# Kernel tuning notes

Hardware: AMD Instinct MI355X
Metric: run time of the kernel (lower is better)

## Reference

```python
import jax, jax.numpy as jnp
import numpy as np

NUM_CLASSES = 15
NUM_ANCHORS = 18          # 3 anchor sizes x 6 angles
STRIDE = 8
SCALE_XY = 1.05


def setup_inputs() -> dict:
    key = jax.random.key(0)
    B, G = 16, 64
    output = jax.random.normal(key, (B, NUM_ANCHORS * (NUM_CLASSES + 6), G, G), dtype=jnp.float32)
    anchors = [(12.0, 16.0), (19.0, 36.0), (40.0, 28.0)]
    angles = [-np.pi / 3, -np.pi / 6, 0.0, np.pi / 6, np.pi / 3, np.pi / 2]
    ma = np.array([(w / STRIDE, h / STRIDE, a) for (w, h) in anchors for a in angles], dtype=np.float32)
    return {"output": output, "masked_anchors": jnp.asarray(ma)}


def reference(output, masked_anchors):
    B, _, G, _ = output.shape
    # [B, nA, G, G, 6+C]
    pred = output.reshape(B, NUM_ANCHORS, NUM_CLASSES + 6, G, G).transpose(0, 1, 3, 4, 2)

    sxy = jnp.asarray(SCALE_XY, output.dtype)
    pred_xy = jax.nn.sigmoid(pred[..., 0:2]) * sxy - (sxy - 1.0) / 2.0
    pred_a = pred[..., 4]
    pred_conf = jax.nn.sigmoid(pred[..., 5])
    pred_cls = jax.nn.sigmoid(pred[..., 6:])

    grid = jnp.arange(G, dtype=output.dtype)
    grid_x = grid[None, None, None, :]   # varies along last axis
    grid_y = grid[None, None, :, None]   # varies along row axis

    a_w = masked_anchors[:, 0][None, :, None, None]
    a_h = masked_anchors[:, 1][None, :, None, None]
    a_a = masked_anchors[:, 2][None, :, None, None]

    bx = pred_xy[..., 0] + grid_x
    by = pred_xy[..., 1] + grid_y
    bw = jnp.exp(pred[..., 2]) * a_w
    bh = jnp.exp(pred[..., 3]) * a_h
    ba = pred_a + a_a

    stride = jnp.asarray(STRIDE, output.dtype)
    boxes = jnp.stack([bx * stride, by * stride, bw * stride, bh * stride, ba], axis=-1)

    out = jnp.concatenate(
        [boxes.reshape(B, -1, 5), pred_conf.reshape(B, -1, 1), pred_cls.reshape(B, -1, NUM_CLASSES)],
        axis=-1,
    )
    return out
```

## Files before the change

kernel.cpp:

```cpp
#include <hip/hip_runtime.h>
#include <math.h>

#define NUM_CLASSES 15
#define NUM_ANCHORS 18
#define NC6 21
#define GRID 64
#define BATCH 16

typedef float f32x4 __attribute__((ext_vector_type(4)));

__device__ __forceinline__ float sigmoidf_fast(float v) {
    return 1.0f / (1.0f + __expf(-v));
}

__launch_bounds__(256)
__global__ void yolo_layer_kernel(const float* __restrict__ in,
                                  const float* __restrict__ anchors,
                                  float* __restrict__ out) {
    const int gid = blockIdx.x;
    const int y   = gid & (GRID - 1);
    const int a   = (gid >> 6) % NUM_ANCHORS;
    const int b   = gid / (GRID * NUM_ANCHORS);

    __shared__ float lds[GRID * NC6];

    const float aw8 = anchors[a * 3 + 0] * 8.0f;
    const float ah8 = anchors[a * 3 + 1] * 8.0f;
    const float aa  = anchors[a * 3 + 2];

    const int base_in  = (b * (NUM_ANCHORS * NC6) + a * NC6) * (GRID * GRID) + y * GRID;
    const int base_out = gid * (GRID * NC6);

    const int   t  = threadIdx.x;
    const float fy = (float)y;

    #pragma unroll
    for (int q0 = 0; q0 < 2; ++q0) {
        int q = q0 * 256 + t;
        if (q < (NC6 * GRID / 4)) {
            int c  = q >> 4;
            int xs = (q & 15) << 2;
            const float* p = in + base_in + c * (GRID * GRID) + xs;
            f32x4 v = __builtin_nontemporal_load(reinterpret_cast<const f32x4*>(p));
            #pragma unroll
            for (int k = 0; k < 4; ++k) {
                float vk = v[k];
                float r;
                if (c >= 5) {
                    r = sigmoidf_fast(vk);
                } else if (c == 0) {
                    r = (sigmoidf_fast(vk) * 1.05f - 0.025f + (float)(xs + k)) * 8.0f;
                } else if (c == 1) {
                    r = (sigmoidf_fast(vk) * 1.05f - 0.025f + fy) * 8.0f;
                } else if (c == 2) {
                    r = __expf(vk) * aw8;
                } else if (c == 3) {
                    r = __expf(vk) * ah8;
                } else {
                    r = vk + aa;
                }
                lds[(xs + k) * NC6 + c] = r;
            }
        }
    }
    __syncthreads();

    #pragma unroll
    for (int q0 = 0; q0 < 2; ++q0) {
        int q = q0 * 256 + t;
        if (q < (NC6 * GRID / 4)) {
            f32x4 v = *reinterpret_cast<const f32x4*>(&lds[q * 4]);
            __builtin_nontemporal_store(v, reinterpret_cast<f32x4*>(out + base_out + q * 4));
        }
    }
}

extern "C" void kernel_launch(void* const* d_in, const int* in_sizes, int n_in,
                              void* d_out, int out_size, void* d_ws, size_t ws_size,
                              hipStream_t stream) {
    const float* in      = (const float*)d_in[0];
    const float* anchors = (const float*)d_in[1];
    float* out           = (float*)d_out;

    const int n_groups = BATCH * NUM_ANCHORS * GRID;
    yolo_layer_kernel<<<dim3(n_groups), dim3(256), 0, stream>>>(in, anchors, out);
}
```

Measured before the change: 40.24 us.

## Give each wavefront its own grid row and drop the block barrier

Each 256-thread block now covers four grid rows, one per 64-lane wavefront. Each wave transposes its row through a private LDS slice, so the block-wide __syncthreads is removed. The grid shrinks fourfold and each lane issues up to six vector loads and stores instead of two. Nontemporal load and store hints are replaced by ordinary accesses. The change depends on LDS ordering within a wave, since there is no explicit barrier between the LDS writes and the reads.

```diff
diff --git a/kernel.cpp b/kernel.cpp
--- a/kernel.cpp
+++ b/kernel.cpp
@@ -17,31 +17,33 @@
 __global__ void yolo_layer_kernel(const float* __restrict__ in,
                                   const float* __restrict__ anchors,
                                   float* __restrict__ out) {
-    const int gid = blockIdx.x;
-    const int y   = gid & (GRID - 1);
-    const int a   = (gid >> 6) % NUM_ANCHORS;
-    const int b   = gid / (GRID * NUM_ANCHORS);
+    const int g  = blockIdx.x;
+    const int y0 = (g & 15) << 2;
+    const int a  = (g >> 4) % NUM_ANCHORS;
+    const int b  = g / (16 * NUM_ANCHORS);
 
-    __shared__ float lds[GRID * NC6];
+    const int w    = threadIdx.x >> 6;
+    const int lane = threadIdx.x & 63;
+    const int y    = y0 + w;
+
+    __shared__ float lds[4][GRID * NC6];
 
     const float aw8 = anchors[a * 3 + 0] * 8.0f;
     const float ah8 = anchors[a * 3 + 1] * 8.0f;
     const float aa  = anchors[a * 3 + 2];
 
     const int base_in  = (b * (NUM_ANCHORS * NC6) + a * NC6) * (GRID * GRID) + y * GRID;
-    const int base_out = gid * (GRID * NC6);
+    const int base_out = ((b * NUM_ANCHORS + a) * (GRID * GRID) + y * GRID) * NC6;
 
-    const int   t  = threadIdx.x;
     const float fy = (float)y;
 
     #pragma unroll
-    for (int q0 = 0; q0 < 2; ++q0) {
-        int q = q0 * 256 + t;
-        if (q < (NC6 * GRID / 4)) {
-            int c  = q >> 4;
-            int xs = (q & 15) << 2;
-            const float* p = in + base_in + c * (GRID * GRID) + xs;
-            f32x4 v = __builtin_nontemporal_load(reinterpret_cast<const f32x4*>(p));
+    for (int i = 0; i < 6; ++i) {
+        int qq = i * 64 + lane;
+        if (qq < (NC6 * GRID / 4)) {
+            int c  = qq >> 4;
+            int xs = (qq & 15) << 2;
+            f32x4 v = *reinterpret_cast<const f32x4*>(in + base_in + c * (GRID * GRID) + xs);
             #pragma unroll
             for (int k = 0; k < 4; ++k) {
                 float vk = v[k];
@@ -59,18 +61,18 @@
                 } else {
                     r = vk + aa;
                 }
-                lds[(xs + k) * NC6 + c] = r;
+                lds[w][(xs + k) * NC6 + c] = r;
             }
         }
     }
-    __syncthreads();
+
 
     #pragma unroll
-    for (int q0 = 0; q0 < 2; ++q0) {
-        int q = q0 * 256 + t;
-        if (q < (NC6 * GRID / 4)) {
-            f32x4 v = *reinterpret_cast<const f32x4*>(&lds[q * 4]);
-            __builtin_nontemporal_store(v, reinterpret_cast<f32x4*>(out + base_out + q * 4));
+    for (int i = 0; i < 6; ++i) {
+        int qq = i * 64 + lane;
+        if (qq < (NC6 * GRID / 4)) {
+            f32x4 v = *reinterpret_cast<const f32x4*>(&lds[w][qq * 4]);
+            *reinterpret_cast<f32x4*>(out + base_out + qq * 4) = v;
         }
     }
 }
@@ -82,6 +84,6 @@
     const float* anchors = (const float*)d_in[1];
     float* out           = (float*)d_out;
 
-    const int n_groups = BATCH * NUM_ANCHORS * GRID;
+    const int n_groups = BATCH * NUM_ANCHORS * (GRID / 4);
     yolo_layer_kernel<<<dim3(n_groups), dim3(256), 0, stream>>>(in, anchors, out);
 }
```

Result: faster. 35.66 us (-11.4%).
